# Kernel optimization log

Measured on AMD Instinct MI355X. Metric: run time of the kernel, lower is better.

The kernel has to match this reference:

```python
import jax, jax.numpy as jnp
import numpy as np

B, L = 8, 12288
MASK_P = 0.01  # sparsity of the label-correlation adjacency


def setup_inputs() -> dict:
    key = jax.random.key(0)
    k1, k2, k3, k4 = jax.random.split(key, 4)
    predicts = jax.random.normal(k1, (B, L), dtype=jnp.float32)
    similarities = jax.random.uniform(k2, (B, B), dtype=jnp.float32)
    adj = jax.random.uniform(k3, (L, L), dtype=jnp.float32)
    adj_mask = jax.random.bernoulli(k4, MASK_P, (L, L))  # bool: lj in adjList[li]
    return {"predicts": predicts, "similarities": similarities,
            "adj": adj, "adj_mask": adj_mask}


def reference(predicts, similarities, adj, adj_mask):
    dt = predicts.dtype
    m = adj_mask.astype(dt)                      # [L, L]
    diag_m = jnp.diagonal(m)                     # [L]
    eye = jnp.eye(adj.shape[0], dtype=dt)
    # effective matrix: masked adjacency weight, else identity on diagonal
    b_eff = m * adj + eye * (1.0 - diag_m)[None, :]
    # relation_num per target label lj
    counts = jnp.sum(m, axis=0) + (1.0 - diag_m)  # [L]
    candidates = (predicts @ b_eff) / counts[None, :]          # [B, L]
    diff = predicts - similarities @ candidates                # [B, L]
    norms = jnp.sqrt(jnp.sum(diff * diff, axis=1))             # [B]
    valid = jnp.sum(similarities, axis=1) != 0                 # [B]
    cnt = jnp.sum(valid.astype(dt))
    total = jnp.sum(jnp.where(valid, norms, jnp.zeros((), dt)))
    return jnp.where(cnt == 0, jnp.zeros((), dt), total / jnp.maximum(cnt, 1.0))
```

## Files before the change

kernel.cpp:

```cpp
#include <hip/hip_runtime.h>
#include <hip/hip_bf16.h>
#include <stdint.h>

#define BB 8
#define LL 12288
#define NCB 6
#define NCH 128
#define RPC (LL / NCH)

#define WS_FLAGS 0
#define WS_NORM2 16
#define WS_SACC  32
#define WS_CNT   (WS_SACC + BB * LL)
#define WS_PART  (WS_CNT + LL)
#define WS_CNTP  (WS_PART + NCH * BB * LL)

__device__ __forceinline__ float bf2f(uint16_t u) {
  union { uint32_t i; float f; } v; v.i = ((uint32_t)u) << 16; return v.f;
}

__device__ __forceinline__ void unpack8(uint4 u, float* f) {
  union { uint32_t i; float v; } t;
  t.i = u.x << 16;          f[0] = t.v;
  t.i = u.x & 0xFFFF0000u;  f[1] = t.v;
  t.i = u.y << 16;          f[2] = t.v;
  t.i = u.y & 0xFFFF0000u;  f[3] = t.v;
  t.i = u.z << 16;          f[4] = t.v;
  t.i = u.z & 0xFFFF0000u;  f[5] = t.v;
  t.i = u.w << 16;          f[6] = t.v;
  t.i = u.w & 0xFFFF0000u;  f[7] = t.v;
}

__global__ void detect_kernel(const uint8_t* __restrict__ mask,
                              const uint8_t* __restrict__ adj,
                              int* __restrict__ flags) {
  __shared__ int s[6];
  int tid = threadIdx.x;
  if (tid < 6) s[tid] = 0;
  __syncthreads();
  int c[4] = {0, 0, 0, 0};
  int big = 0, hi = 0;
  const int N = 65536;
  for (int idx = tid; idx < N; idx += blockDim.x) {
    uint8_t v = mask[idx];
    if (v) { c[idx & 3]++; if (v >= 2) big++; }
    uint8_t a = adj[idx];
    if ((idx & 3) == 1 && a >= 0x80) hi++;
  }
  atomicAdd(&s[0], c[0]); atomicAdd(&s[1], c[1]);
  atomicAdd(&s[2], c[2]); atomicAdd(&s[3], c[3]);
  atomicAdd(&s[4], big);  atomicAdd(&s[5], hi);
  __syncthreads();
  if (tid == 0) {
    int width;
    int nzoff = s[1] + s[2] + s[3];
    if (nzoff == 0)             width = 4;
    else if (s[0] + s[1] == 0)  width = 4;
    else if (s[4] == 0)         width = 1;
    else                        width = 2;
    flags[0] = width;
    flags[1] = (s[5] == 0) ? 1 : 0;
  }
}

template <int MW, int FB>
__device__ void s1loop(const uint8_t* __restrict__ mask,
                       const uint8_t* __restrict__ adj,
                       float* __restrict__ part, float* __restrict__ cntp,
                       const float* __restrict__ sp,
                       int j0, int i0, int ch) {
  float acc[BB][8];
  float c8[8] = {0.f, 0.f, 0.f, 0.f, 0.f, 0.f, 0.f, 0.f};
#pragma unroll
  for (int b = 0; b < BB; b++)
#pragma unroll
    for (int k = 0; k < 8; k++) acc[b][k] = 0.f;

#pragma unroll 2
  for (int il = 0; il < RPC; ++il) {
    size_t e = (size_t)(i0 + il) * LL + j0;
    float a[8];
    if (FB) {
      uint4 u = *reinterpret_cast<const uint4*>(adj + e * 2);
      unpack8(u, a);
    } else {
      float4 f0 = *reinterpret_cast<const float4*>(adj + e * 4);
      float4 f1 = *reinterpret_cast<const float4*>(adj + e * 4 + 16);
      a[0] = f0.x; a[1] = f0.y; a[2] = f0.z; a[3] = f0.w;
      a[4] = f1.x; a[5] = f1.y; a[6] = f1.z; a[7] = f1.w;
    }
    int m[8];
    if (MW == 1) {
      uint2 u = *reinterpret_cast<const uint2*>(mask + e);
      m[0] = (u.x & 0x000000FFu) != 0; m[1] = (u.x & 0x0000FF00u) != 0;
      m[2] = (u.x & 0x00FF0000u) != 0; m[3] = (u.x & 0xFF000000u) != 0;
      m[4] = (u.y & 0x000000FFu) != 0; m[5] = (u.y & 0x0000FF00u) != 0;
      m[6] = (u.y & 0x00FF0000u) != 0; m[7] = (u.y & 0xFF000000u) != 0;
    } else if (MW == 2) {
      uint4 u = *reinterpret_cast<const uint4*>(mask + e * 2);
      m[0] = (u.x & 0xFFFFu) != 0; m[1] = (u.x >> 16) != 0;
      m[2] = (u.y & 0xFFFFu) != 0; m[3] = (u.y >> 16) != 0;
      m[4] = (u.z & 0xFFFFu) != 0; m[5] = (u.z >> 16) != 0;
      m[6] = (u.w & 0xFFFFu) != 0; m[7] = (u.w >> 16) != 0;
    } else {
      uint4 u0 = *reinterpret_cast<const uint4*>(mask + e * 4);
      uint4 u1 = *reinterpret_cast<const uint4*>(mask + e * 4 + 16);
      m[0] = u0.x != 0; m[1] = u0.y != 0; m[2] = u0.z != 0; m[3] = u0.w != 0;
      m[4] = u1.x != 0; m[5] = u1.y != 0; m[6] = u1.z != 0; m[7] = u1.w != 0;
    }
#pragma unroll
    for (int k = 0; k < 8; k++) {
      a[k] = m[k] ? a[k] : 0.f;
      c8[k] += m[k] ? 1.f : 0.f;
    }
    float4 p0 = *reinterpret_cast<const float4*>(sp + il * BB);
    float4 p1 = *reinterpret_cast<const float4*>(sp + il * BB + 4);
    float pv[BB] = {p0.x, p0.y, p0.z, p0.w, p1.x, p1.y, p1.z, p1.w};
#pragma unroll
    for (int b = 0; b < BB; b++)
#pragma unroll
      for (int k = 0; k < 8; k++) acc[b][k] = fmaf(pv[b], a[k], acc[b][k]);
  }
#pragma unroll
  for (int b = 0; b < BB; b++) {
    float* dst = part + ((size_t)ch * BB + b) * LL + j0;
    *reinterpret_cast<float4*>(dst)     = make_float4(acc[b][0], acc[b][1], acc[b][2], acc[b][3]);
    *reinterpret_cast<float4*>(dst + 4) = make_float4(acc[b][4], acc[b][5], acc[b][6], acc[b][7]);
  }
  float* cdst = cntp + (size_t)ch * LL + j0;
  *reinterpret_cast<float4*>(cdst)     = make_float4(c8[0], c8[1], c8[2], c8[3]);
  *reinterpret_cast<float4*>(cdst + 4) = make_float4(c8[4], c8[5], c8[6], c8[7]);
}

__global__ __launch_bounds__(256) void stage1(const uint8_t* __restrict__ mask,
                                              const uint8_t* __restrict__ adj,
                                              const uint8_t* __restrict__ pred,
                                              float* __restrict__ ws) {
  __shared__ float sp[RPC * BB];
  const int* fl = (const int*)ws;
  int mw = fl[0], fb = fl[1];
  int cb = blockIdx.x % NCB;
  int ch = blockIdx.x / NCB;
  int j0 = cb * 2048 + threadIdx.x * 8;
  int i0 = ch * RPC;
  for (int idx = threadIdx.x; idx < RPC * BB; idx += 256) {
    int b = idx / RPC, il = idx % RPC;
    float p = fb ? bf2f(reinterpret_cast<const uint16_t*>(pred)[b * LL + i0 + il])
                 : reinterpret_cast<const float*>(pred)[b * LL + i0 + il];
    sp[il * BB + b] = p;
  }
  __syncthreads();
  float* part = ws + WS_PART;
  float* cntp = ws + WS_CNTP;
  if (fb) {
    if (mw == 1)      s1loop<1, 1>(mask, adj, part, cntp, sp, j0, i0, ch);
    else if (mw == 2) s1loop<2, 1>(mask, adj, part, cntp, sp, j0, i0, ch);
    else              s1loop<4, 1>(mask, adj, part, cntp, sp, j0, i0, ch);
  } else {
    if (mw == 1)      s1loop<1, 0>(mask, adj, part, cntp, sp, j0, i0, ch);
    else if (mw == 2) s1loop<2, 0>(mask, adj, part, cntp, sp, j0, i0, ch);
    else              s1loop<4, 0>(mask, adj, part, cntp, sp, j0, i0, ch);
  }
}

__global__ __launch_bounds__(256) void reduce_kernel(float* __restrict__ ws) {
  int idx = blockIdx.x * 256 + threadIdx.x;
  const float* part = ws + WS_PART;
  float s = 0.f;
#pragma unroll 8
  for (int c = 0; c < NCH; c++) s += part[(size_t)c * (BB * LL) + idx];
  ws[WS_SACC + idx] = s;
  if (idx < LL) {
    const float* cntp = ws + WS_CNTP;
    float cs = 0.f;
#pragma unroll 8
    for (int c = 0; c < NCH; c++) cs += cntp[(size_t)c * LL + idx];
    ws[WS_CNT + idx] = cs;
  }
}

__global__ __launch_bounds__(256) void stage23(const uint8_t* __restrict__ mask,
                                               const uint8_t* __restrict__ pred,
                                               const uint8_t* __restrict__ sim,
                                               float* __restrict__ ws) {
  const int* fl = (const int*)ws;
  int mw = fl[0], fb = fl[1];
  float* sacc = ws + WS_SACC;
  float* cntw = ws + WS_CNT;
  float* norm2 = ws + WS_NORM2;
  __shared__ float ssim[64];
  if (threadIdx.x < 64) {
    ssim[threadIdx.x] = fb ? bf2f(((const uint16_t*)sim)[threadIdx.x])
                           : ((const float*)sim)[threadIdx.x];
  }
  __syncthreads();
  int j = blockIdx.x * 256 + threadIdx.x;
  size_t ed = (size_t)j * LL + j;
  int mjj;
  if (mw == 1)      mjj = mask[ed] != 0;
  else if (mw == 2) mjj = ((const uint16_t*)mask)[ed] != 0;
  else              mjj = ((const uint32_t*)mask)[ed] != 0;
  float add = mjj ? 0.f : 1.f;
  float c = cntw[j] + add;
  float pj[BB], cv[BB];
#pragma unroll
  for (int b = 0; b < BB; b++)
    pj[b] = fb ? bf2f(((const uint16_t*)pred)[b * LL + j])
               : ((const float*)pred)[b * LL + j];
#pragma unroll
  for (int k = 0; k < BB; k++) cv[k] = (sacc[k * LL + j] + pj[k] * add) / c;
#pragma unroll
  for (int b = 0; b < BB; b++) {
    float t = pj[b];
#pragma unroll
    for (int k = 0; k < BB; k++) t = fmaf(-ssim[b * 8 + k], cv[k], t);
    float v = t * t;
#pragma unroll
    for (int off = 32; off > 0; off >>= 1) v += __shfl_down(v, off, 64);
    if ((threadIdx.x & 63) == 0) unsafeAtomicAdd(&norm2[b], v);
  }
}

__global__ void stage4(const uint8_t* __restrict__ sim,
                       uint8_t* __restrict__ out, float* __restrict__ ws) {
  if (threadIdx.x != 0) return;
  const int* fl = (const int*)ws;
  int fb = fl[1];
  float* norm2 = ws + WS_NORM2;
  float total = 0.f, cntv = 0.f;
  for (int b = 0; b < BB; b++) {
    float rs = 0.f;
    for (int k = 0; k < 8; k++)
      rs += fb ? bf2f(((const uint16_t*)sim)[b * 8 + k])
               : ((const float*)sim)[b * 8 + k];
    if (rs != 0.f) { cntv += 1.f; total += sqrtf(norm2[b]); }
  }
  float res = (cntv == 0.f) ? 0.f : total / fmaxf(cntv, 1.f);
  if (fb) *reinterpret_cast<__hip_bfloat16*>(out) = __float2bfloat16(res);
  else    *reinterpret_cast<float*>(out) = res;
}

extern "C" void kernel_launch(void* const* d_in, const int* in_sizes, int n_in,
                              void* d_out, int out_size, void* d_ws,
                              size_t ws_size, hipStream_t stream) {
  const uint8_t* pred = (const uint8_t*)d_in[0];
  const uint8_t* sim  = (const uint8_t*)d_in[1];
  const uint8_t* adj  = (const uint8_t*)d_in[2];
  const uint8_t* mask = (const uint8_t*)d_in[3];
  float* ws = (float*)d_ws;

  hipMemsetAsync(d_ws, 0, 32 * sizeof(float), stream);
  detect_kernel<<<1, 256, 0, stream>>>(mask, adj, (int*)d_ws);
  stage1<<<NCB * NCH, 256, 0, stream>>>(mask, adj, pred, ws);
  reduce_kernel<<<BB * LL / 256, 256, 0, stream>>>(ws);
  stage23<<<LL / 256, 256, 0, stream>>>(mask, pred, sim, ws);
  stage4<<<1, 64, 0, stream>>>(sim, (uint8_t*)d_out, ws);
}
```

Before: 1.389 ms.

## Skip adjacency loads when mask group is empty and narrow per-thread column tile

Each thread now handles 4 columns instead of 8, with twice as many column blocks and half as many row chunks. It reads the mask first and loads the adjacency values only when at least one of its 4 mask entries is set. At 1% mask density most adjacency reads can be skipped, which cuts memory traffic on the dominant input. In exchange, the adjacency load depends on the mask load and the branch can diverge within a wavefront, and the partial-sum buffer shrinks because there are fewer row chunks.

```diff
diff --git a/kernel.cpp b/kernel.cpp
--- a/kernel.cpp
+++ b/kernel.cpp
@@ -4,8 +4,8 @@
 
 #define BB 8
 #define LL 12288
-#define NCB 6
-#define NCH 128
+#define NCB 12
+#define NCH 64
 #define RPC (LL / NCH)
 
 #define WS_FLAGS 0
@@ -17,18 +17,6 @@
 
 __device__ __forceinline__ float bf2f(uint16_t u) {
   union { uint32_t i; float f; } v; v.i = ((uint32_t)u) << 16; return v.f;
-}
-
-__device__ __forceinline__ void unpack8(uint4 u, float* f) {
-  union { uint32_t i; float v; } t;
-  t.i = u.x << 16;          f[0] = t.v;
-  t.i = u.x & 0xFFFF0000u;  f[1] = t.v;
-  t.i = u.y << 16;          f[2] = t.v;
-  t.i = u.y & 0xFFFF0000u;  f[3] = t.v;
-  t.i = u.z << 16;          f[4] = t.v;
-  t.i = u.z & 0xFFFF0000u;  f[5] = t.v;
-  t.i = u.w << 16;          f[6] = t.v;
-  t.i = u.w & 0xFFFF0000u;  f[7] = t.v;
 }
 
 __global__ void detect_kernel(const uint8_t* __restrict__ mask,
@@ -69,49 +57,51 @@
                        float* __restrict__ part, float* __restrict__ cntp,
                        const float* __restrict__ sp,
                        int j0, int i0, int ch) {
-  float acc[BB][8];
-  float c8[8] = {0.f, 0.f, 0.f, 0.f, 0.f, 0.f, 0.f, 0.f};
+  float acc[BB][4];
+  float c4[4] = {0.f, 0.f, 0.f, 0.f};
 #pragma unroll
   for (int b = 0; b < BB; b++)
 #pragma unroll
-    for (int k = 0; k < 8; k++) acc[b][k] = 0.f;
+    for (int k = 0; k < 4; k++) acc[b][k] = 0.f;
 
 #pragma unroll 2
   for (int il = 0; il < RPC; ++il) {
     size_t e = (size_t)(i0 + il) * LL + j0;
-    float a[8];
-    if (FB) {
-      uint4 u = *reinterpret_cast<const uint4*>(adj + e * 2);
-      unpack8(u, a);
-    } else {
-      float4 f0 = *reinterpret_cast<const float4*>(adj + e * 4);
-      float4 f1 = *reinterpret_cast<const float4*>(adj + e * 4 + 16);
-      a[0] = f0.x; a[1] = f0.y; a[2] = f0.z; a[3] = f0.w;
-      a[4] = f1.x; a[5] = f1.y; a[6] = f1.z; a[7] = f1.w;
-    }
-    int m[8];
+    int m[4];
     if (MW == 1) {
-      uint2 u = *reinterpret_cast<const uint2*>(mask + e);
-      m[0] = (u.x & 0x000000FFu) != 0; m[1] = (u.x & 0x0000FF00u) != 0;
-      m[2] = (u.x & 0x00FF0000u) != 0; m[3] = (u.x & 0xFF000000u) != 0;
-      m[4] = (u.y & 0x000000FFu) != 0; m[5] = (u.y & 0x0000FF00u) != 0;
-      m[6] = (u.y & 0x00FF0000u) != 0; m[7] = (u.y & 0xFF000000u) != 0;
+      uint32_t u = *reinterpret_cast<const uint32_t*>(mask + e);
+      m[0] = (u & 0x000000FFu) != 0; m[1] = (u & 0x0000FF00u) != 0;
+      m[2] = (u & 0x00FF0000u) != 0; m[3] = (u & 0xFF000000u) != 0;
     } else if (MW == 2) {
-      uint4 u = *reinterpret_cast<const uint4*>(mask + e * 2);
+      uint2 u = *reinterpret_cast<const uint2*>(mask + e * 2);
       m[0] = (u.x & 0xFFFFu) != 0; m[1] = (u.x >> 16) != 0;
       m[2] = (u.y & 0xFFFFu) != 0; m[3] = (u.y >> 16) != 0;
-      m[4] = (u.z & 0xFFFFu) != 0; m[5] = (u.z >> 16) != 0;
-      m[6] = (u.w & 0xFFFFu) != 0; m[7] = (u.w >> 16) != 0;
     } else {
-      uint4 u0 = *reinterpret_cast<const uint4*>(mask + e * 4);
-      uint4 u1 = *reinterpret_cast<const uint4*>(mask + e * 4 + 16);
-      m[0] = u0.x != 0; m[1] = u0.y != 0; m[2] = u0.z != 0; m[3] = u0.w != 0;
-      m[4] = u1.x != 0; m[5] = u1.y != 0; m[6] = u1.z != 0; m[7] = u1.w != 0;
+      uint4 u = *reinterpret_cast<const uint4*>(mask + e * 4);
+      m[0] = u.x != 0; m[1] = u.y != 0; m[2] = u.z != 0; m[3] = u.w != 0;
     }
-#pragma unroll
-    for (int k = 0; k < 8; k++) {
+    int any = m[0] | m[1] | m[2] | m[3];
+
+    float a[4] = {0.f, 0.f, 0.f, 0.f};
+    if (FB) {
+      if (any) {
+        uint2 u = *reinterpret_cast<const uint2*>(adj + e * 2);
+        union { uint32_t i; float v; } t;
+        t.i = u.x << 16;          a[0] = t.v;
+        t.i = u.x & 0xFFFF0000u;  a[1] = t.v;
+        t.i = u.y << 16;          a[2] = t.v;
+        t.i = u.y & 0xFFFF0000u;  a[3] = t.v;
+      }
+    } else {
+      if (any) {
+        float4 f = *reinterpret_cast<const float4*>(adj + e * 4);
+        a[0] = f.x; a[1] = f.y; a[2] = f.z; a[3] = f.w;
+      }
+    }
+#pragma unroll
+    for (int k = 0; k < 4; k++) {
       a[k] = m[k] ? a[k] : 0.f;
-      c8[k] += m[k] ? 1.f : 0.f;
+      c4[k] += m[k] ? 1.f : 0.f;
     }
     float4 p0 = *reinterpret_cast<const float4*>(sp + il * BB);
     float4 p1 = *reinterpret_cast<const float4*>(sp + il * BB + 4);
@@ -119,17 +109,16 @@
 #pragma unroll
     for (int b = 0; b < BB; b++)
 #pragma unroll
-      for (int k = 0; k < 8; k++) acc[b][k] = fmaf(pv[b], a[k], acc[b][k]);
+      for (int k = 0; k < 4; k++) acc[b][k] = fmaf(pv[b], a[k], acc[b][k]);
   }
 #pragma unroll
   for (int b = 0; b < BB; b++) {
     float* dst = part + ((size_t)ch * BB + b) * LL + j0;
-    *reinterpret_cast<float4*>(dst)     = make_float4(acc[b][0], acc[b][1], acc[b][2], acc[b][3]);
-    *reinterpret_cast<float4*>(dst + 4) = make_float4(acc[b][4], acc[b][5], acc[b][6], acc[b][7]);
+    *reinterpret_cast<float4*>(dst) =
+        make_float4(acc[b][0], acc[b][1], acc[b][2], acc[b][3]);
   }
   float* cdst = cntp + (size_t)ch * LL + j0;
-  *reinterpret_cast<float4*>(cdst)     = make_float4(c8[0], c8[1], c8[2], c8[3]);
-  *reinterpret_cast<float4*>(cdst + 4) = make_float4(c8[4], c8[5], c8[6], c8[7]);
+  *reinterpret_cast<float4*>(cdst) = make_float4(c4[0], c4[1], c4[2], c4[3]);
 }
 
 __global__ __launch_bounds__(256) void stage1(const uint8_t* __restrict__ mask,
@@ -141,7 +130,7 @@
   int mw = fl[0], fb = fl[1];
   int cb = blockIdx.x % NCB;
   int ch = blockIdx.x / NCB;
-  int j0 = cb * 2048 + threadIdx.x * 8;
+  int j0 = cb * 1024 + threadIdx.x * 4;
   int i0 = ch * RPC;
   for (int idx = threadIdx.x; idx < RPC * BB; idx += 256) {
     int b = idx / RPC, il = idx % RPC;
```

New measurement: 1.315 ms. 1.06x faster.
